# Kernel optimization log

Hardware: AMD Instinct MI355X
Metric: run time of the kernel (lower is better)

The kernel has to match this reference:

```python
import jax, jax.numpy as jnp
import numpy as np

# KroneckerLinear: W ~= sum_i (A_i kron B_i); efficient path computes, per token,
# Y = sum_i A_i @ X @ B_i^T with X = x.reshape(in1, in2), output flattened as (out1*out2).

IN1, IN2 = 64, 64      # in_factors (in1*in2 = in_features = 4096)
OUT1, OUT2 = 64, 64    # out_factors (out1*out2 = out_features = 4096)
NUM_SUM = 2
BATCH, SEQ = 4, 4096


def setup_inputs() -> dict:
    key = jax.random.key(0)
    kx, ka, kb, kbias = jax.random.split(key, 4)
    x = jax.random.normal(kx, (BATCH, SEQ, IN1 * IN2), dtype=jnp.float32)
    # kaiming-uniform-like scale for small factors
    bound_a = 1.0 / np.sqrt(IN1)
    bound_b = 1.0 / np.sqrt(IN2)
    A = jax.random.uniform(ka, (NUM_SUM, OUT1, IN1), dtype=jnp.float32, minval=-bound_a, maxval=bound_a)
    B = jax.random.uniform(kb, (NUM_SUM, OUT2, IN2), dtype=jnp.float32, minval=-bound_b, maxval=bound_b)
    bound = 1.0 / np.sqrt(IN1 * IN2)
    bias = jax.random.uniform(kbias, (OUT1 * OUT2,), dtype=jnp.float32, minval=-bound, maxval=bound)
    return {"x": x, "A": A, "B": B, "bias": bias}


def reference(x, A, B, bias):
    Bsz, T, _ = x.shape
    X = x.reshape(Bsz, T, IN1, IN2)  # (b, t, i, j)
    # y[b,t,o,p] = sum_s sum_ij A[s,o,i] * X[b,t,i,j] * B[s,p,j]  -> (out1, out2)
    y = jnp.einsum("btij,soi,spj->btop", X, A, B)
    return y.reshape(Bsz, T, OUT1 * OUT2) + bias
```

## Files before the change

kernel.cpp:

```cpp
#include <hip/hip_runtime.h>

typedef float  f32x4  __attribute__((ext_vector_type(4)));
typedef short  bf16x8 __attribute__((ext_vector_type(8)));

#define NT       16384
#define NBLOCK   256
#define NSTREAM  1024
#define TPS      16

__device__ __forceinline__ short f2bf(float x) {
  unsigned u = __builtin_bit_cast(unsigned, x);
  u = (u + 0x7FFFu + ((u >> 16) & 1u)) >> 16;
  return (short)u;
}

__device__ __forceinline__ void gload16(const float* gp, float* lp) {
  __builtin_amdgcn_global_load_lds((const __attribute__((address_space(1))) void*)gp,
                                   (__attribute__((address_space(3))) void*)lp,
                                   16, 0, 0);
}

__device__ __forceinline__ void stage(float* XB, const float* gbase, int lane) {
#pragma unroll
  for (int q = 0; q < 16; ++q) {
    const int i  = q * 4 + (lane >> 4);
    const int qp = lane & 15;
    const float* gp = gbase + i * 64 + ((qp ^ (i & 7)) << 2);
    gload16(gp, XB + q * 256);
  }
}

__device__ __forceinline__ void body(float* XB,
                                     const bf16x8* AT, const bf16x8* BT,
                                     int tok, bool pf, int lane, int g, int l15,
                                     const float* __restrict__ x,
                                     const float* __restrict__ bias,
                                     float* __restrict__ out) {
  asm volatile("s_waitcnt vmcnt(48)" ::: "memory");

  const f32x4* xb4 = (const f32x4*)XB;

  bf16x8 xf[4][2];
#pragma unroll
  for (int it = 0; it < 4; ++it) {
#pragma unroll
    for (int jc = 0; jc < 2; ++jc) {
      const int i  = it * 16 + l15;
      const int q0 = jc * 8 + 2 * g;
      f32x4 f0 = xb4[i * 16 + ((q0    ) ^ (i & 7))];
      f32x4 f1 = xb4[i * 16 + ((q0 + 1) ^ (i & 7))];
      bf16x8 t;
      t[0]=f2bf(f0.x); t[1]=f2bf(f0.y); t[2]=f2bf(f0.z); t[3]=f2bf(f0.w);
      t[4]=f2bf(f1.x); t[5]=f2bf(f1.y); t[6]=f2bf(f1.z); t[7]=f2bf(f1.w);
      xf[it][jc] = t;
    }
  }

  f32x4 acc2[4][4];
#pragma unroll
  for (int a = 0; a < 4; ++a)
#pragma unroll
    for (int b = 0; b < 4; ++b)
      acc2[a][b] = (f32x4){0.f, 0.f, 0.f, 0.f};

#pragma unroll
  for (int s = 0; s < 2; ++s) {
    bf16x8 bfr[4][2];
#pragma unroll
    for (int pt = 0; pt < 4; ++pt)
#pragma unroll
      for (int jc = 0; jc < 2; ++jc)
        bfr[pt][jc] = BT[(s * 8 + pt * 2 + jc) * 64 + lane];

    f32x4 a1[4][4];
#pragma unroll
    for (int a = 0; a < 4; ++a)
#pragma unroll
      for (int b = 0; b < 4; ++b)
        a1[a][b] = (f32x4){0.f, 0.f, 0.f, 0.f};
#pragma unroll
    for (int it = 0; it < 4; ++it)
#pragma unroll
      for (int pt = 0; pt < 4; ++pt)
#pragma unroll
        for (int jc = 0; jc < 2; ++jc)
          a1[it][pt] = __builtin_amdgcn_mfma_f32_16x16x32_bf16(
              xf[it][jc], bfr[pt][jc], a1[it][pt], 0, 0, 0);

    bf16x8 uf[4][2];
#pragma unroll
    for (int pt = 0; pt < 4; ++pt)
#pragma unroll
      for (int c = 0; c < 2; ++c) {
        bf16x8 t;
#pragma unroll
        for (int e = 0; e < 8; ++e)
          t[e] = f2bf(a1[(e >> 2) + 2 * c][pt][e & 3]);
        uf[pt][c] = t;
      }

    bf16x8 afr[4][2];
#pragma unroll
    for (int ot = 0; ot < 4; ++ot)
#pragma unroll
      for (int c = 0; c < 2; ++c)
        afr[ot][c] = AT[(s * 8 + ot * 2 + c) * 64 + lane];

#pragma unroll
    for (int pt = 0; pt < 4; ++pt)
#pragma unroll
      for (int ot = 0; ot < 4; ++ot)
#pragma unroll
        for (int c = 0; c < 2; ++c)
          acc2[pt][ot] = __builtin_amdgcn_mfma_f32_16x16x32_bf16(
              uf[pt][c], afr[ot][c], acc2[pt][ot], 0, 0, 0);
  }

  const int pcol = 4 * g;
  f32x4 bv[4][4];
#pragma unroll
  for (int pt = 0; pt < 4; ++pt)
#pragma unroll
    for (int ot = 0; ot < 4; ++ot)
      bv[pt][ot] = *(const f32x4*)(bias + (ot * 16 + l15) * 64 + pt * 16 + pcol);

  asm volatile("" ::: "memory");
  if (pf) stage(XB, x + ((size_t)(tok + 2 * NSTREAM) << 12), lane);
  asm volatile("" ::: "memory");

  float* ob = out + ((size_t)tok << 12);
#pragma unroll
  for (int pt = 0; pt < 4; ++pt)
#pragma unroll
    for (int ot = 0; ot < 4; ++ot) {
      f32x4 r = acc2[pt][ot] + bv[pt][ot];
      *(f32x4*)(ob + (ot * 16 + l15) * 64 + pt * 16 + pcol) = r;
    }
}

__global__ __launch_bounds__(256) void kron_kernel(const float* __restrict__ x,
                                                   const float* __restrict__ A,
                                                   const float* __restrict__ B,
                                                   const float* __restrict__ bias,
                                                   float* __restrict__ out) {
  __shared__ float  xb[4][2][4096];
  __shared__ bf16x8 AT[1024];
  __shared__ bf16x8 BT[1024];

  const int lane = threadIdx.x & 63;
  const int w    = threadIdx.x >> 6;
  const int g    = lane >> 4;
  const int l15  = lane & 15;
  const int sid  = blockIdx.x * 4 + w;

#pragma unroll
  for (int t = 0; t < 4; ++t) {
    const int idx = w * 4 + t;
    const int s = idx >> 3, ot = (idx & 7) >> 1, c = idx & 1;
    const int o = ot * 16 + l15;
    bf16x8 v;
#pragma unroll
    for (int e = 0; e < 8; ++e) {
      const int i = c * 32 + 4 * g + (e & 3) + 16 * (e >> 2);
      v[e] = f2bf(A[s * 4096 + o * 64 + i]);
    }
    AT[idx * 64 + lane] = v;
  }
#pragma unroll
  for (int t = 0; t < 4; ++t) {
    const int idx = w * 4 + t;
    const int s = idx >> 3, pt = (idx & 7) >> 1, jc = idx & 1;
    const int p = pt * 16 + l15;
    bf16x8 v;
#pragma unroll
    for (int e = 0; e < 8; ++e) {
      const int j = jc * 32 + 8 * g + e;
      v[e] = f2bf(B[s * 4096 + p * 64 + j]);
    }
    BT[idx * 64 + lane] = v;
  }
  __syncthreads();

  float* xb0 = &xb[w][0][0];
  float* xb1 = &xb[w][1][0];

  stage(xb0, x + ((size_t)sid << 12), lane);
  stage(xb1, x + ((size_t)(sid + NSTREAM) << 12), lane);
  asm volatile("s_waitcnt vmcnt(16)" ::: "memory");

  for (int k = 0; k < TPS; k += 2) {
    body(xb0, AT, BT, sid + NSTREAM * k,       k + 2 < TPS, lane, g, l15, x, bias, out);
    body(xb1, AT, BT, sid + NSTREAM * (k + 1), k + 3 < TPS, lane, g, l15, x, bias, out);
  }
}

extern "C" void kernel_launch(void* const* d_in, const int* in_sizes, int n_in,
                              void* d_out, int out_size, void* d_ws, size_t ws_size,
                              hipStream_t stream) {
  const float* x    = (const float*)d_in[0];
  const float* A    = (const float*)d_in[1];
  const float* B    = (const float*)d_in[2];
  const float* bias = (const float*)d_in[3];
  float* out        = (float*)d_out;
  kron_kernel<<<dim3(NBLOCK), dim3(256), 0, stream>>>(x, A, B, bias, out);
}
```

Baseline: 123.9 us.

## Replace LDS async staging with register prefetch of next token

Drops the per-wave LDS double buffer filled by global_load_lds. Each wave now loads the next token's X tile straight into registers while computing the current token, then converts it to bf16 after the stores. The grid doubles to 512 blocks, each wave processes a contiguous run of tokens, and launch bounds now request 2 blocks per CU. This frees 128KB of LDS per block to allow more occupancy, at the cost of higher register pressure and loss of the explicit vmcnt-controlled deep prefetch.

```diff
diff --git a/kernel.cpp b/kernel.cpp
--- a/kernel.cpp
+++ b/kernel.cpp
@@ -3,10 +3,11 @@
 typedef float  f32x4  __attribute__((ext_vector_type(4)));
 typedef short  bf16x8 __attribute__((ext_vector_type(8)));
 
-#define NT       16384
-#define NBLOCK   256
-#define NSTREAM  1024
-#define TPS      16
+#define NT      16384
+#define NBLOCK  512
+#define WPB     4
+#define NSTREAM (NBLOCK * WPB)
+#define TPS     (NT / NSTREAM)
 
 __device__ __forceinline__ short f2bf(float x) {
   unsigned u = __builtin_bit_cast(unsigned, x);
@@ -14,136 +15,11 @@
   return (short)u;
 }
 
-__device__ __forceinline__ void gload16(const float* gp, float* lp) {
-  __builtin_amdgcn_global_load_lds((const __attribute__((address_space(1))) void*)gp,
-                                   (__attribute__((address_space(3))) void*)lp,
-                                   16, 0, 0);
-}
-
-__device__ __forceinline__ void stage(float* XB, const float* gbase, int lane) {
-#pragma unroll
-  for (int q = 0; q < 16; ++q) {
-    const int i  = q * 4 + (lane >> 4);
-    const int qp = lane & 15;
-    const float* gp = gbase + i * 64 + ((qp ^ (i & 7)) << 2);
-    gload16(gp, XB + q * 256);
-  }
-}
-
-__device__ __forceinline__ void body(float* XB,
-                                     const bf16x8* AT, const bf16x8* BT,
-                                     int tok, bool pf, int lane, int g, int l15,
-                                     const float* __restrict__ x,
-                                     const float* __restrict__ bias,
-                                     float* __restrict__ out) {
-  asm volatile("s_waitcnt vmcnt(48)" ::: "memory");
-
-  const f32x4* xb4 = (const f32x4*)XB;
-
-  bf16x8 xf[4][2];
-#pragma unroll
-  for (int it = 0; it < 4; ++it) {
-#pragma unroll
-    for (int jc = 0; jc < 2; ++jc) {
-      const int i  = it * 16 + l15;
-      const int q0 = jc * 8 + 2 * g;
-      f32x4 f0 = xb4[i * 16 + ((q0    ) ^ (i & 7))];
-      f32x4 f1 = xb4[i * 16 + ((q0 + 1) ^ (i & 7))];
-      bf16x8 t;
-      t[0]=f2bf(f0.x); t[1]=f2bf(f0.y); t[2]=f2bf(f0.z); t[3]=f2bf(f0.w);
-      t[4]=f2bf(f1.x); t[5]=f2bf(f1.y); t[6]=f2bf(f1.z); t[7]=f2bf(f1.w);
-      xf[it][jc] = t;
-    }
-  }
-
-  f32x4 acc2[4][4];
-#pragma unroll
-  for (int a = 0; a < 4; ++a)
-#pragma unroll
-    for (int b = 0; b < 4; ++b)
-      acc2[a][b] = (f32x4){0.f, 0.f, 0.f, 0.f};
-
-#pragma unroll
-  for (int s = 0; s < 2; ++s) {
-    bf16x8 bfr[4][2];
-#pragma unroll
-    for (int pt = 0; pt < 4; ++pt)
-#pragma unroll
-      for (int jc = 0; jc < 2; ++jc)
-        bfr[pt][jc] = BT[(s * 8 + pt * 2 + jc) * 64 + lane];
-
-    f32x4 a1[4][4];
-#pragma unroll
-    for (int a = 0; a < 4; ++a)
-#pragma unroll
-      for (int b = 0; b < 4; ++b)
-        a1[a][b] = (f32x4){0.f, 0.f, 0.f, 0.f};
-#pragma unroll
-    for (int it = 0; it < 4; ++it)
-#pragma unroll
-      for (int pt = 0; pt < 4; ++pt)
-#pragma unroll
-        for (int jc = 0; jc < 2; ++jc)
-          a1[it][pt] = __builtin_amdgcn_mfma_f32_16x16x32_bf16(
-              xf[it][jc], bfr[pt][jc], a1[it][pt], 0, 0, 0);
-
-    bf16x8 uf[4][2];
-#pragma unroll
-    for (int pt = 0; pt < 4; ++pt)
-#pragma unroll
-      for (int c = 0; c < 2; ++c) {
-        bf16x8 t;
-#pragma unroll
-        for (int e = 0; e < 8; ++e)
-          t[e] = f2bf(a1[(e >> 2) + 2 * c][pt][e & 3]);
-        uf[pt][c] = t;
-      }
-
-    bf16x8 afr[4][2];
-#pragma unroll
-    for (int ot = 0; ot < 4; ++ot)
-#pragma unroll
-      for (int c = 0; c < 2; ++c)
-        afr[ot][c] = AT[(s * 8 + ot * 2 + c) * 64 + lane];
-
-#pragma unroll
-    for (int pt = 0; pt < 4; ++pt)
-#pragma unroll
-      for (int ot = 0; ot < 4; ++ot)
-#pragma unroll
-        for (int c = 0; c < 2; ++c)
-          acc2[pt][ot] = __builtin_amdgcn_mfma_f32_16x16x32_bf16(
-              uf[pt][c], afr[ot][c], acc2[pt][ot], 0, 0, 0);
-  }
-
-  const int pcol = 4 * g;
-  f32x4 bv[4][4];
-#pragma unroll
-  for (int pt = 0; pt < 4; ++pt)
-#pragma unroll
-    for (int ot = 0; ot < 4; ++ot)
-      bv[pt][ot] = *(const f32x4*)(bias + (ot * 16 + l15) * 64 + pt * 16 + pcol);
-
-  asm volatile("" ::: "memory");
-  if (pf) stage(XB, x + ((size_t)(tok + 2 * NSTREAM) << 12), lane);
-  asm volatile("" ::: "memory");
-
-  float* ob = out + ((size_t)tok << 12);
-#pragma unroll
-  for (int pt = 0; pt < 4; ++pt)
-#pragma unroll
-    for (int ot = 0; ot < 4; ++ot) {
-      f32x4 r = acc2[pt][ot] + bv[pt][ot];
-      *(f32x4*)(ob + (ot * 16 + l15) * 64 + pt * 16 + pcol) = r;
-    }
-}
-
-__global__ __launch_bounds__(256) void kron_kernel(const float* __restrict__ x,
-                                                   const float* __restrict__ A,
-                                                   const float* __restrict__ B,
-                                                   const float* __restrict__ bias,
-                                                   float* __restrict__ out) {
-  __shared__ float  xb[4][2][4096];
+__global__ __launch_bounds__(256, 2) void kron_kernel(const float* __restrict__ x,
+                                                      const float* __restrict__ A,
+                                                      const float* __restrict__ B,
+                                                      const float* __restrict__ bias,
+                                                      float* __restrict__ out) {
   __shared__ bf16x8 AT[1024];
   __shared__ bf16x8 BT[1024];
 
@@ -151,7 +27,7 @@
   const int w    = threadIdx.x >> 6;
   const int g    = lane >> 4;
   const int l15  = lane & 15;
-  const int sid  = blockIdx.x * 4 + w;
+  const int sid  = blockIdx.x * WPB + w;
 
 #pragma unroll
   for (int t = 0; t < 4; ++t) {
@@ -181,16 +57,113 @@
   }
   __syncthreads();
 
-  float* xb0 = &xb[w][0][0];
-  float* xb1 = &xb[w][1][0];
+  const float* xs = x + ((size_t)sid * TPS << 12);
 
-  stage(xb0, x + ((size_t)sid << 12), lane);
-  stage(xb1, x + ((size_t)(sid + NSTREAM) << 12), lane);
-  asm volatile("s_waitcnt vmcnt(16)" ::: "memory");
+  f32x4 xr[4][2][2];
+  auto loadX = [&](int kk) {
+    const float* xb = xs + ((size_t)kk << 12);
+#pragma unroll
+    for (int it = 0; it < 4; ++it)
+#pragma unroll
+      for (int jc = 0; jc < 2; ++jc) {
+        const float* p = xb + (16 * it + l15) * 64 + 32 * jc + 8 * g;
+        xr[it][jc][0] = *(const f32x4*)p;
+        xr[it][jc][1] = *(const f32x4*)(p + 4);
+      }
+  };
 
-  for (int k = 0; k < TPS; k += 2) {
-    body(xb0, AT, BT, sid + NSTREAM * k,       k + 2 < TPS, lane, g, l15, x, bias, out);
-    body(xb1, AT, BT, sid + NSTREAM * (k + 1), k + 3 < TPS, lane, g, l15, x, bias, out);
+  bf16x8 xf[4][2];
+  auto convX = [&]() {
+#pragma unroll
+    for (int it = 0; it < 4; ++it)
+#pragma unroll
+      for (int jc = 0; jc < 2; ++jc) {
+        f32x4 f0 = xr[it][jc][0], f1 = xr[it][jc][1];
+        bf16x8 t;
+        t[0]=f2bf(f0.x); t[1]=f2bf(f0.y); t[2]=f2bf(f0.z); t[3]=f2bf(f0.w);
+        t[4]=f2bf(f1.x); t[5]=f2bf(f1.y); t[6]=f2bf(f1.z); t[7]=f2bf(f1.w);
+        xf[it][jc] = t;
+      }
+  };
+
+  loadX(0);
+  convX();
+
+  for (int k = 0; k < TPS; ++k) {
+    if (k + 1 < TPS) loadX(k + 1);
+
+    f32x4 acc2[4][4];
+#pragma unroll
+    for (int a = 0; a < 4; ++a)
+#pragma unroll
+      for (int b = 0; b < 4; ++b)
+        acc2[a][b] = (f32x4){0.f, 0.f, 0.f, 0.f};
+
+#pragma unroll
+    for (int s = 0; s < 2; ++s) {
+      bf16x8 bfr[4][2];
+#pragma unroll
+      for (int pt = 0; pt < 4; ++pt)
+#pragma unroll
+        for (int jc = 0; jc < 2; ++jc)
+          bfr[pt][jc] = BT[(s * 8 + pt * 2 + jc) * 64 + lane];
+
+      f32x4 a1[4][4];
+#pragma unroll
+      for (int a = 0; a < 4; ++a)
+#pragma unroll
+        for (int b = 0; b < 4; ++b)
+          a1[a][b] = (f32x4){0.f, 0.f, 0.f, 0.f};
+#pragma unroll
+      for (int it = 0; it < 4; ++it)
+#pragma unroll
+        for (int pt = 0; pt < 4; ++pt)
+#pragma unroll
+          for (int jc = 0; jc < 2; ++jc)
+            a1[it][pt] = __builtin_amdgcn_mfma_f32_16x16x32_bf16(
+                xf[it][jc], bfr[pt][jc], a1[it][pt], 0, 0, 0);
+
+      bf16x8 uf[4][2];
+#pragma unroll
+      for (int pt = 0; pt < 4; ++pt)
+#pragma unroll
+        for (int c = 0; c < 2; ++c) {
+          bf16x8 t;
+#pragma unroll
+          for (int e = 0; e < 8; ++e)
+            t[e] = f2bf(a1[(e >> 2) + 2 * c][pt][e & 3]);
+          uf[pt][c] = t;
+        }
+
+      bf16x8 afr[4][2];
+#pragma unroll
+      for (int ot = 0; ot < 4; ++ot)
+#pragma unroll
+        for (int c = 0; c < 2; ++c)
+          afr[ot][c] = AT[(s * 8 + ot * 2 + c) * 64 + lane];
+
+#pragma unroll
+      for (int pt = 0; pt < 4; ++pt)
+#pragma unroll
+        for (int ot = 0; ot < 4; ++ot)
+#pragma unroll
+          for (int c = 0; c < 2; ++c)
+            acc2[pt][ot] = __builtin_amdgcn_mfma_f32_16x16x32_bf16(
+                uf[pt][c], afr[ot][c], acc2[pt][ot], 0, 0, 0);
+    }
+
+    const int pcol = 4 * g;
+    float* ob = out + (((size_t)sid * TPS + k) << 12);
+#pragma unroll
+    for (int pt = 0; pt < 4; ++pt)
+#pragma unroll
+      for (int ot = 0; ot < 4; ++ot) {
+        const int off = (ot * 16 + l15) * 64 + pt * 16 + pcol;
+        f32x4 bv = *(const f32x4*)(bias + off);
+        *(f32x4*)(ob + off) = acc2[pt][ot] + bv;
+      }
+
+    if (k + 1 < TPS) convX();
   }
 }
 
```

After: 289.7 us. +133.9%, slower.
